# Kernel optimization log

Hardware: AMD Instinct MI355X
Metric: run time of the kernel (lower is better)

Reference implementation:

```python
import jax, jax.numpy as jnp
import numpy as np

WINDOW = (2, 7, 7)
SHIFT = (1, 3, 3)
HEADS = 4


def _rel_pos_index(ws):
    coords = np.stack(np.meshgrid(*[np.arange(w) for w in ws], indexing='ij'))  # (3, wd, wh, ww)
    cf = coords.reshape(3, -1)
    rel = cf[:, :, None] - cf[:, None, :]  # (3, N, N)
    rel = rel.transpose(1, 2, 0).astype(np.int64)
    rel[:, :, 0] += ws[0] - 1
    rel[:, :, 1] += ws[1] - 1
    rel[:, :, 2] += ws[2] - 1
    rel[:, :, 0] *= (2 * ws[1] - 1) * (2 * ws[2] - 1)
    rel[:, :, 1] *= 2 * ws[2] - 1
    return rel.sum(-1)  # (N, N)


def _attn_mask(D, H, W, ws, ss):
    img = np.zeros((1, D, H, W, 1), np.float32)
    cnt = 0
    for d in (slice(None, -ws[0]), slice(-ws[0], -ss[0]), slice(-ss[0], None)):
        for h in (slice(None, -ws[1]), slice(-ws[1], -ss[1]), slice(-ss[1], None)):
            for w in (slice(None, -ws[2]), slice(-ws[2], -ss[2]), slice(-ss[2], None)):
                img[:, d, h, w, :] = cnt
                cnt += 1
    N = ws[0] * ws[1] * ws[2]
    mw = img.reshape(1, D // ws[0], ws[0], H // ws[1], ws[1], W // ws[2], ws[2], 1)
    mw = mw.transpose(0, 1, 3, 5, 2, 4, 6, 7).reshape(-1, N)  # (nW, N)
    diff = mw[:, None, :] - mw[:, :, None]
    return np.where(diff != 0, -100.0, 0.0).astype(np.float32)  # (nW, N, N)


def _win_partition(x, ws):
    B, D, H, W, C = x.shape
    x = x.reshape(B, D // ws[0], ws[0], H // ws[1], ws[1], W // ws[2], ws[2], C)
    return x.transpose(0, 1, 3, 5, 2, 4, 6, 7).reshape(-1, ws[0] * ws[1] * ws[2], C)


def _win_reverse(win, ws, B, D, H, W):
    C = win.shape[-1]
    x = win.reshape(B, D // ws[0], H // ws[1], W // ws[2], ws[0], ws[1], ws[2], C)
    return x.transpose(0, 1, 4, 2, 5, 3, 6, 7).reshape(B, D, H, W, C)


def _ln(x, w, b):
    mu = x.mean(-1, keepdims=True)
    var = x.var(-1, keepdims=True)
    return (x - mu) / jnp.sqrt(var + 1e-5) * w + b


def setup_inputs() -> dict:
    key = jax.random.key(0)
    ks = jax.random.split(key, 8)
    B, D, H, W, C = 4, 8, 56, 56, 128
    hidden = 4 * C
    table = (2 * WINDOW[0] - 1) * (2 * WINDOW[1] - 1) * (2 * WINDOW[2] - 1)
    return {
        'x': jax.random.normal(ks[0], (B, D, H, W, C), jnp.float32),
        'norm1_w': jnp.ones((C,), jnp.float32),
        'norm1_b': jnp.zeros((C,), jnp.float32),
        'qkv_w': 0.02 * jax.random.normal(ks[1], (3 * C, C), jnp.float32),
        'qkv_b': jnp.zeros((3 * C,), jnp.float32),
        'rpb': 0.02 * jax.random.normal(ks[2], (table, HEADS), jnp.float32),
        'proj_w': 0.02 * jax.random.normal(ks[3], (C, C), jnp.float32),
        'proj_b': jnp.zeros((C,), jnp.float32),
        'norm2_w': jnp.ones((C,), jnp.float32),
        'norm2_b': jnp.zeros((C,), jnp.float32),
        'fc1_w': 0.02 * jax.random.normal(ks[4], (hidden, C), jnp.float32),
        'fc1_b': jnp.zeros((hidden,), jnp.float32),
        'fc2_w': 0.02 * jax.random.normal(ks[5], (C, hidden), jnp.float32),
        'fc2_b': jnp.zeros((C,), jnp.float32),
    }


def reference(x, norm1_w, norm1_b, qkv_w, qkv_b, rpb, proj_w, proj_b,
              norm2_w, norm2_b, fc1_w, fc1_b, fc2_w, fc2_b):
    B, D, H, W, C = x.shape
    hd = C // HEADS
    scale = hd ** -0.5
    N = WINDOW[0] * WINDOW[1] * WINDOW[2]

    shortcut = x
    y = _ln(x, norm1_w, norm1_b)
    # cyclic shift (SW-MSA)
    y = jnp.roll(y, (-SHIFT[0], -SHIFT[1], -SHIFT[2]), axis=(1, 2, 3))
    win = _win_partition(y, WINDOW)  # (B_, N, C)
    B_ = win.shape[0]

    qkv = win @ qkv_w.T + qkv_b  # (B_, N, 3C)
    qkv = qkv.reshape(B_, N, 3, HEADS, hd).transpose(2, 0, 3, 1, 4)
    q, k, v = qkv[0] * scale, qkv[1], qkv[2]  # (B_, h, N, hd)

    attn = jnp.einsum('bhnd,bhmd->bhnm', q, k)  # (B_, h, N, N)
    rpi = _rel_pos_index(WINDOW)
    bias = rpb[rpi.reshape(-1)].reshape(N, N, HEADS).transpose(2, 0, 1)  # (h, N, N)
    attn = attn + bias[None]

    mask = jnp.asarray(_attn_mask(D, H, W, WINDOW, SHIFT))  # (nW, N, N)
    nW = mask.shape[0]
    attn = attn.reshape(B_ // nW, nW, HEADS, N, N) + mask[None, :, None]
    attn = jax.nn.softmax(attn.reshape(B_, HEADS, N, N), axis=-1)

    out = jnp.einsum('bhnm,bhmd->bhnd', attn, v)
    out = out.transpose(0, 2, 1, 3).reshape(B_, N, C)
    out = out @ proj_w.T + proj_b

    y = _win_reverse(out, WINDOW, B, D, H, W)
    y = jnp.roll(y, SHIFT, axis=(1, 2, 3))  # reverse cyclic shift
    x = shortcut + y

    h = _ln(x, norm2_w, norm2_b)
    h = jax.nn.gelu(h @ fc1_w.T + fc1_b, approximate=False)
    h = h @ fc2_w.T + fc2_b
    return x + h
```

## Files before the change

kernel.cpp:

```cpp
#include <hip/hip_runtime.h>
#include <math.h>

typedef short bf16x8 __attribute__((ext_vector_type(8)));
typedef float f32x4 __attribute__((ext_vector_type(4)));
typedef unsigned short u16;

#define DEVFN static __device__ __forceinline__

DEVFN u16 f2bf(float f) {
  union { float f; unsigned u; } v; v.f = f;
  return (u16)((v.u + 0x7FFFu + ((v.u >> 16) & 1u)) >> 16);
}

DEVFN void gload16(const void* g, void* l) {
  __builtin_amdgcn_global_load_lds(
      (const __attribute__((address_space(1))) void*)g,
      (__attribute__((address_space(3))) void*)l, 16, 0, 0);
}

DEVFN float gelu_tanh(float x) {
  float x2 = x * x;
  float m = x * fmaf(0.044715f, x2, 1.0f);
  float e = __expf(-1.5957691216057308f * m);
  return x / (1.0f + e);
}

#define TT 100352
#define BWIN 1024

__global__ void convert4_kernel(const float* __restrict__ a, const float* __restrict__ b,
                                const float* __restrict__ c, const float* __restrict__ d,
                                u16* __restrict__ oa, u16* __restrict__ ob,
                                u16* __restrict__ oc, u16* __restrict__ od) {
  int i = blockIdx.x * 256 + threadIdx.x;
  const float* s; u16* o; int off;
  if (i < 49152)       { s = a; o = oa; off = i; }
  else if (i < 65536)  { s = b; o = ob; off = i - 49152; }
  else if (i < 131072) { s = c; o = oc; off = i - 65536; }
  else                 { s = d; o = od; off = i - 131072; }
  o[off] = f2bf(s[off]);
}

__global__ void bias_kernel(const float* __restrict__ rpb, float* __restrict__ bias_full) {
  int idx = blockIdx.x * 256 + threadIdx.x;
  if (idx >= 4 * 9604) return;
  int h = idx / 9604, rem = idx % 9604, i = rem / 98, j = rem % 98;
  int di = i / 49, ri = i % 49, hi = ri / 7, wi = ri % 7;
  int dj = j / 49, rj = j % 49, hj = rj / 7, wj = rj % 7;
  int tidx = (di - dj + 1) * 169 + (hi - hj + 6) * 13 + (wi - wj + 6);
  bias_full[idx] = rpb[tidx * 4 + h];
}

template<int SHIFTED>
__global__ __launch_bounds__(256) void ln_kernel(const float* __restrict__ x,
    const float* __restrict__ w, const float* __restrict__ bterm, u16* __restrict__ out)
{
  int gw = blockIdx.x * 4 + (threadIdx.x >> 6);
  int lane = threadIdx.x & 63;
  size_t src;
  if (SHIFTED) {
    int b_ = gw / 98, n = gw % 98;
    int bb = b_ >> 8, widx = b_ & 255;
    int dw = widx >> 6, hw = (widx >> 3) & 7, ww = widx & 7;
    int dd = n / 49, rr = n % 49, hh = rr / 7, wn = rr % 7;
    int d = (dw * 2 + dd + 1) & 7;
    int h = hw * 7 + hh + 3; if (h >= 56) h -= 56;
    int wq = ww * 7 + wn + 3; if (wq >= 56) wq -= 56;
    src = ((size_t)(((bb * 8 + d) * 56 + h) * 56 + wq)) * 128;
  } else {
    src = (size_t)gw * 128;
  }
  float2 v = *(const float2*)(x + src + lane * 2);
  float s = v.x + v.y, q = v.x * v.x + v.y * v.y;
  #pragma unroll
  for (int m = 1; m < 64; m <<= 1) { s += __shfl_xor(s, m, 64); q += __shfl_xor(q, m, 64); }
  float mu = s * (1.0f / 128.0f);
  float var = q * (1.0f / 128.0f) - mu * mu;
  float rstd = rsqrtf(var + 1e-5f);
  int c = lane * 2;
  float y0 = (v.x - mu) * rstd * w[c] + bterm[c];
  float y1 = (v.y - mu) * rstd * w[c + 1] + bterm[c + 1];
  ushort2 o; o.x = f2bf(y0); o.y = f2bf(y1);
  *(ushort2*)(out + (size_t)gw * 128 + c) = o;
}

template<int EPI>
__global__ __launch_bounds__(256) void gemm_kernel(
    const u16* __restrict__ A, const u16* __restrict__ Bw,
    const float* __restrict__ bias, const float* __restrict__ res,
    void* __restrict__ outp, int M, int N, int K)
{
  __shared__ u16 smem[16384];
  u16* As = smem;
  u16* Bs = smem + 8192;
  const int m0 = blockIdx.x * 128, n0 = blockIdx.y * 128;
  const int t = threadIdx.x;
  const int wid = t >> 6, lane = t & 63;
  const int wr = wid >> 1, wc = wid & 1;
  const int l15 = lane & 15, lhi = lane >> 4;
  const int srow = lane >> 3;
  const int sslot = lane & 7;
  const int gcol = ((sslot ^ srow) << 3);
  f32x4 acc[4][4] = {};
  for (int k0 = 0; k0 < K; k0 += 64) {
    #pragma unroll
    for (int it = 0; it < 4; ++it) {
      const int rbase = it * 32 + wid * 8;
      const int row = rbase + srow;
      gload16(A + (size_t)(m0 + row) * K + k0 + gcol, As + rbase * 64);
      gload16(Bw + (size_t)(n0 + row) * K + k0 + gcol, Bs + rbase * 64);
    }
    __syncthreads();
    #pragma unroll
    for (int kk = 0; kk < 64; kk += 32) {
      bf16x8 af[4], bfr[4];
      const int csw = (kk + lhi * 8) ^ ((l15 & 7) << 3);
      #pragma unroll
      for (int mi = 0; mi < 4; ++mi) af[mi] = *(const bf16x8*)(As + (wr * 64 + mi * 16 + l15) * 64 + csw);
      #pragma unroll
      for (int ni = 0; ni < 4; ++ni) bfr[ni] = *(const bf16x8*)(Bs + (wc * 64 + ni * 16 + l15) * 64 + csw);
      #pragma unroll
      for (int mi = 0; mi < 4; ++mi)
        #pragma unroll
        for (int ni = 0; ni < 4; ++ni)
          acc[mi][ni] = __builtin_amdgcn_mfma_f32_16x16x32_bf16(af[mi], bfr[ni], acc[mi][ni], 0, 0, 0);
    }
    __syncthreads();
  }
  if (EPI == 0) {
    const float smul = (n0 == 0) ? 0.17677669529663689f : 1.0f;
    #pragma unroll
    for (int mi = 0; mi < 4; ++mi)
      #pragma unroll
      for (int ni = 0; ni < 4; ++ni) {
        int col = wc * 64 + ni * 16 + l15;
        float bcol = bias[n0 + col];
        #pragma unroll
        for (int r = 0; r < 4; ++r) {
          int row = wr * 64 + mi * 16 + lhi * 4 + r;
          float v = (acc[mi][ni][r] + bcol) * smul;
          smem[row * 128 + (((col >> 3) ^ (row & 7)) << 3) + (col & 7)] = f2bf(v);
        }
      }
    __syncthreads();
    const int rsub = t >> 4, sl = t & 15;
    #pragma unroll
    for (int j = 0; j < 8; ++j) {
      int row = j * 16 + rsub;
      int4 val = *(const int4*)(smem + row * 128 + ((sl ^ (row & 7)) << 3));
      *(int4*)((u16*)outp + (size_t)(m0 + row) * N + n0 + sl * 8) = val;
    }
  } else {
    #pragma unroll
    for (int mi = 0; mi < 4; ++mi)
      #pragma unroll
      for (int r = 0; r < 4; ++r) {
        int row = m0 + wr * 64 + mi * 16 + lhi * 4 + r;
        int b_ = row / 98, n = row % 98;
        int bb = b_ >> 8, widx = b_ & 255;
        int dw = widx >> 6, hw = (widx >> 3) & 7, ww = widx & 7;
        int dd = n / 49, rr = n % 49, hh = rr / 7, wn = rr % 7;
        int d = (dw * 2 + dd + 1) & 7;
        int h = hw * 7 + hh + 3; if (h >= 56) h -= 56;
        int wq = ww * 7 + wn + 3; if (wq >= 56) wq -= 56;
        size_t dbase = ((size_t)(((bb * 8 + d) * 56 + h) * 56 + wq)) * 128;
        #pragma unroll
        for (int ni = 0; ni < 4; ++ni) {
          int col = n0 + wc * 64 + ni * 16 + l15;
          float v = acc[mi][ni][r] + bias[col];
          ((float*)outp)[dbase + col] = res[dbase + col] + v;
        }
      }
  }
}

__global__ __launch_bounds__(256, 2) void mlp_kernel(
    const u16* __restrict__ A, const u16* __restrict__ W1, const float* __restrict__ b1,
    const u16* __restrict__ W2, const float* __restrict__ b2,
    const float* __restrict__ res, float* __restrict__ outp)
{
  __shared__ u16 smem[38400];
  u16* W1c = smem;
  u16* W2c = smem + 16384;
  u16* HsA = smem + 32768;
  float* b1s = (float*)(smem + 37376);
  float* Pk = (float*)smem;
  const int m0 = blockIdx.x * 64;
  const int t = threadIdx.x, wid = t >> 6, lane = t & 63;
  const int l15 = lane & 15, lhi = lane >> 4;
  const int srow4 = lane >> 4, sslot16 = lane & 15;
  const int srow8 = lane >> 3, sslot8 = lane & 7;
  u16* hs = HsA + wid * 16 * 72;

  #pragma unroll
  for (int it = 0; it < 4; ++it) {
    int rb1 = it * 16 + wid * 4, r1 = rb1 + srow4;
    gload16(W1 + (size_t)r1 * 128 + ((sslot16 ^ (r1 & 7)) << 3), W1c + rb1 * 128);
    int rb2 = it * 32 + wid * 8, r2 = rb2 + srow8;
    gload16(W2 + (size_t)r2 * 512 + ((sslot8 ^ (r2 & 7)) << 3), W2c + rb2 * 64);
  }
  if (t < 128) *(f32x4*)(b1s + t * 4) = *(const f32x4*)(b1 + t * 4);
  bf16x8 areg[4];
  #pragma unroll
  for (int kg = 0; kg < 4; ++kg)
    areg[kg] = *(const bf16x8*)(A + (size_t)(m0 + wid * 16 + l15) * 128 + kg * 32 + lhi * 8);

  f32x4 accO[8] = {};
  __syncthreads();
  for (int hc = 0; hc < 8; ++hc) {
    const int cur = (hc & 1) * 8192;
    if (hc < 7) {
      const int nxt = ((hc + 1) & 1) * 8192;
      #pragma unroll
      for (int it = 0; it < 4; ++it) {
        int rb1 = it * 16 + wid * 4, r1 = rb1 + srow4;
        gload16(W1 + (size_t)((hc + 1) * 64 + r1) * 128 + ((sslot16 ^ (r1 & 7)) << 3),
                W1c + nxt + rb1 * 128);
      }
      #pragma unroll
      for (int it = 0; it < 4; ++it) {
        int rb2 = it * 32 + wid * 8, r2 = rb2 + srow8;
        gload16(W2 + (size_t)r2 * 512 + (hc + 1) * 64 + ((sslot8 ^ (r2 & 7)) << 3),
                W2c + nxt + rb2 * 64);
      }
    }
    f32x4 accH[4] = {};
    #pragma unroll
    for (int kk = 0; kk < 4; ++kk) {
      bf16x8 bfr[4];
      #pragma unroll
      for (int ni = 0; ni < 4; ++ni) {
        int row = ni * 16 + l15;
        bfr[ni] = *(const bf16x8*)(W1c + cur + row * 128 + (((kk * 4 + lhi) ^ (row & 7)) << 3));
      }
      #pragma unroll
      for (int ni = 0; ni < 4; ++ni)
        accH[ni] = __builtin_amdgcn_mfma_f32_16x16x32_bf16(areg[kk], bfr[ni], accH[ni], 0, 0, 0);
    }
    #pragma unroll
    for (int ni = 0; ni < 4; ++ni) {
      float bb = b1s[hc * 64 + ni * 16 + l15];
      #pragma unroll
      for (int r = 0; r < 4; ++r)
        hs[(lhi * 4 + r) * 72 + ni * 16 + l15] = f2bf(gelu_tanh(accH[ni][r] + bb));
    }
    #pragma unroll
    for (int kk = 0; kk < 2; ++kk) {
      bf16x8 ah = *(const bf16x8*)(hs + l15 * 72 + kk * 32 + lhi * 8);
      bf16x8 bfr[8];
      #pragma unroll
      for (int ni = 0; ni < 8; ++ni) {
        int row = ni * 16 + l15;
        bfr[ni] = *(const bf16x8*)(W2c + cur + row * 64 + (((kk * 4 + lhi) ^ (row & 7)) << 3));
      }
      #pragma unroll
      for (int ni = 0; ni < 8; ++ni)
        accO[ni] = __builtin_amdgcn_mfma_f32_16x16x32_bf16(ah, bfr[ni], accO[ni], 0, 0, 0);
    }
    __syncthreads();
  }
  #pragma unroll
  for (int ni = 0; ni < 8; ++ni) {
    int col = ni * 16 + l15;
    float bv = b2[col];
    #pragma unroll
    for (int r = 0; r < 4; ++r)
      Pk[(wid * 16 + lhi * 4 + r) * 132 + col] = accO[ni][r] + bv;
  }
  __syncthreads();
  #pragma unroll
  for (int p = 0; p < 8; ++p) {
    int idx = p * 256 + t;
    int row = idx >> 5, c = (idx & 31) * 4;
    f32x4 v = *(const f32x4*)(Pk + row * 132 + c);
    f32x4 rv = *(const f32x4*)(res + (size_t)(m0 + row) * 128 + c);
    *(f32x4*)(outp + (size_t)(m0 + row) * 128 + c) = v + rv;
  }
}

__global__ __launch_bounds__(64) void attn_kernel(
    const u16* __restrict__ qkv, const float* __restrict__ bias_full,
    u16* __restrict__ out_win)
{
  __shared__ u16 vT[32][136];
  __shared__ u16 P[16][136];
  __shared__ signed char rids[112];
  const int bid = blockIdx.x;
  const int w = bid >> 2, h = bid & 3;
  const int lane = threadIdx.x;
  const int l15 = lane & 15, lhi = lane >> 4;
  const int widx = w & 255;
  const int dw = widx >> 6, hw = (widx >> 3) & 7, ww = widx & 7;

  #pragma unroll
  for (int rep = 0; rep < 2; ++rep) {
    int t2 = lane + rep * 64;
    if (t2 < 112) {
      int rv = 0;
      if (t2 < 98) {
        int dd = t2 / 49, rr = t2 % 49, hh = rr / 7, wn = rr % 7;
        int dp = dw * 2 + dd, hp = hw * 7 + hh, wp = ww * 7 + wn;
        int rd = dp < 6 ? 0 : (dp < 7 ? 1 : 2);
        int rh = hp < 49 ? 0 : (hp < 53 ? 1 : 2);
        int rw2 = wp < 49 ? 0 : (wp < 53 ? 1 : 2);
        rv = rd * 9 + rh * 3 + rw2;
      }
      rids[t2] = (signed char)rv;
    }
  }
  for (int f = lane; f < 160; f += 64) {
    int d = f / 5, c = 96 + (f % 5) * 8;
    *(int4*)&vT[d][c] = (int4){0, 0, 0, 0};
  }
  if (lane < 48) {
    int r = lane / 3, c = 112 + (lane % 3) * 8;
    *(int4*)&P[r][c] = (int4){0, 0, 0, 0};
  }
  const size_t base = (size_t)w * 98 * 384;
  for (int f = lane; f < 392; f += 64) {
    int n = f >> 2, c = (f & 3) * 8;
    int4 v = *(const int4*)(qkv + base + (size_t)n * 384 + 256 + h * 32 + c);
    const u16* pv = (const u16*)&v;
    #pragma unroll
    for (int j = 0; j < 8; ++j) vT[c + j][n] = pv[j];
  }
  __syncthreads();

  const float* bh = bias_full + h * 9604;
  const size_t obase = (size_t)w * 98 * 128;
  for (int mt = 0; mt < 7; ++mt) {
    int qn = mt * 16 + l15; if (qn > 97) qn = 97;
    bf16x8 aq = *(const bf16x8*)(qkv + base + (size_t)qn * 384 + h * 32 + lhi * 8);
    f32x4 sf[7];
    #pragma unroll
    for (int nt = 0; nt < 7; ++nt) {
      int kn = nt * 16 + l15; if (kn > 97) kn = 97;
      bf16x8 bk = *(const bf16x8*)(qkv + base + (size_t)kn * 384 + 128 + h * 32 + lhi * 8);
      f32x4 z = {0.f, 0.f, 0.f, 0.f};
      sf[nt] = __builtin_amdgcn_mfma_f32_16x16x32_bf16(aq, bk, z, 0, 0, 0);
    }
    int irow[4], ridr[4];
    #pragma unroll
    for (int r = 0; r < 4; ++r) {
      irow[r] = mt * 16 + lhi * 4 + r;
      ridr[r] = rids[irow[r] > 111 ? 111 : irow[r]];
    }
    float mx[4] = {-1e30f, -1e30f, -1e30f, -1e30f};
    #pragma unroll
    for (int nt = 0; nt < 7; ++nt) {
      int j = nt * 16 + l15;
      int jc = j > 97 ? 97 : j;
      int rj = rids[j];
      #pragma unroll
      for (int r = 0; r < 4; ++r) {
        float s = sf[nt][r];
        int ic = irow[r] > 97 ? 97 : irow[r];
        s += bh[ic * 98 + jc];
        if (ridr[r] != rj) s -= 100.0f;
        if (j > 97) s = -1e30f;
        sf[nt][r] = s;
        mx[r] = fmaxf(mx[r], s);
      }
    }
    #pragma unroll
    for (int m = 1; m < 16; m <<= 1)
      #pragma unroll
      for (int r = 0; r < 4; ++r) mx[r] = fmaxf(mx[r], __shfl_xor(mx[r], m, 64));
    float sm[4] = {0.f, 0.f, 0.f, 0.f};
    #pragma unroll
    for (int nt = 0; nt < 7; ++nt)
      #pragma unroll
      for (int r = 0; r < 4; ++r) {
        float p = __expf(sf[nt][r] - mx[r]);
        sf[nt][r] = p;
        sm[r] += p;
      }
    #pragma unroll
    for (int m = 1; m < 16; m <<= 1)
      #pragma unroll
      for (int r = 0; r < 4; ++r) sm[r] += __shfl_xor(sm[r], m, 64);
    float inv[4];
    #pragma unroll
    for (int r = 0; r < 4; ++r) inv[r] = 1.0f / sm[r];
    __syncthreads();
    #pragma unroll
    for (int nt = 0; nt < 7; ++nt)
      #pragma unroll
      for (int r = 0; r < 4; ++r)
        P[lhi * 4 + r][nt * 16 + l15] = f2bf(sf[nt][r] * inv[r]);
    __syncthreads();
    f32x4 o0 = {}, o1 = {};
    #pragma unroll
    for (int ks = 0; ks < 4; ++ks) {
      bf16x8 ap  = *(const bf16x8*)(&P[l15][ks * 32 + lhi * 8]);
      bf16x8 bv0 = *(const bf16x8*)(&vT[l15][ks * 32 + lhi * 8]);
      bf16x8 bv1 = *(const bf16x8*)(&vT[16 + l15][ks * 32 + lhi * 8]);
      o0 = __builtin_amdgcn_mfma_f32_16x16x32_bf16(ap, bv0, o0, 0, 0, 0);
      o1 = __builtin_amdgcn_mfma_f32_16x16x32_bf16(ap, bv1, o1, 0, 0, 0);
    }
    #pragma unroll
    for (int r = 0; r < 4; ++r) {
      if (irow[r] < 98) {
        size_t orow = obase + (size_t)irow[r] * 128 + h * 32;
        out_win[orow + l15] = f2bf(o0[r]);
        out_win[orow + 16 + l15] = f2bf(o1[r]);
      }
    }
  }
}

extern "C" void kernel_launch(void* const* d_in, const int* in_sizes, int n_in,
                              void* d_out, int out_size, void* d_ws, size_t ws_size,
                              hipStream_t stream)
{
  const float* x      = (const float*)d_in[0];
  const float* n1w    = (const float*)d_in[1];
  const float* n1b    = (const float*)d_in[2];
  const float* qkv_w  = (const float*)d_in[3];
  const float* qkv_b  = (const float*)d_in[4];
  const float* rpb    = (const float*)d_in[5];
  const float* proj_w = (const float*)d_in[6];
  const float* proj_b = (const float*)d_in[7];
  const float* n2w    = (const float*)d_in[8];
  const float* n2b    = (const float*)d_in[9];
  const float* fc1_w  = (const float*)d_in[10];
  const float* fc1_b  = (const float*)d_in[11];
  const float* fc2_w  = (const float*)d_in[12];
  const float* fc2_b  = (const float*)d_in[13];

  char* p = (char*)d_ws;
  size_t off = 0;
  auto alloc = [&](size_t bytes) { void* r = p + off; off = (off + bytes + 255) & ~(size_t)255; return r; };
  u16*   qkvw_b    = (u16*)alloc(49152 * 2);
  u16*   projw_b   = (u16*)alloc(16384 * 2);
  u16*   fc1w_b    = (u16*)alloc(65536 * 2);
  u16*   fc2w_b    = (u16*)alloc(65536 * 2);
  float* bias_full = (float*)alloc(4 * 9604 * 4);
  u16*   y_win     = (u16*)alloc((size_t)TT * 128 * 2);
  float* x2        = (float*)alloc((size_t)TT * 128 * 4);
  u16*   h1        = (u16*)alloc((size_t)TT * 128 * 2);
  u16*   big       = (u16*)alloc((size_t)TT * 384 * 2);
  if (off > ws_size) return;

  convert4_kernel<<<768, 256, 0, stream>>>(qkv_w, proj_w, fc1_w, fc2_w,
                                           qkvw_b, projw_b, fc1w_b, fc2w_b);
  bias_kernel<<<(4 * 9604 + 255) / 256, 256, 0, stream>>>(rpb, bias_full);
  ln_kernel<1><<<TT / 4, 256, 0, stream>>>(x, n1w, n1b, y_win);
  gemm_kernel<0><<<dim3(TT / 128, 3), 256, 0, stream>>>(y_win, qkvw_b, qkv_b, nullptr, big, TT, 384, 128);
  attn_kernel<<<BWIN * 4, 64, 0, stream>>>(big, bias_full, y_win);
  gemm_kernel<1><<<dim3(TT / 128, 1), 256, 0, stream>>>(y_win, projw_b, proj_b, x, x2, TT, 128, 128);
  ln_kernel<0><<<TT / 4, 256, 0, stream>>>(x2, n2w, n2b, h1);
  mlp_kernel<<<TT / 64, 256, 0, stream>>>(h1, fc1w_b, fc1_b, fc2w_b, fc2_b, x2, (float*)d_out);
}
```

Measured before the change: 234.3 us.

## Double MLP token tile to 128 rows, single-buffer W1, use sigmoid GELU

The fused MLP kernel now handles 128 tokens per block, with each wave owning 32 rows, so every W1/W2 chunk staged in LDS feeds twice as many MFMAs and the grid is halved. To keep LDS small, W1 is single-buffered and its next chunk is prefetched only after a barrier that follows the first GEMM, while W2 stays double-buffered. The epilogue writes the output in two 64-row halves through the same LDS staging area. GELU switches from the tanh form to the cheaper x*sigmoid(1.702x) form using a hardware reciprocal, which is less accurate against the exact erf GELU. The risks are the extra barrier, higher register pressure from doubled accumulators, and less latency hiding on W1.

```diff
diff --git a/kernel.cpp b/kernel.cpp
--- a/kernel.cpp
+++ b/kernel.cpp
@@ -18,11 +18,9 @@
       (__attribute__((address_space(3))) void*)l, 16, 0, 0);
 }
 
-DEVFN float gelu_tanh(float x) {
-  float x2 = x * x;
-  float m = x * fmaf(0.044715f, x2, 1.0f);
-  float e = __expf(-1.5957691216057308f * m);
-  return x / (1.0f + e);
+DEVFN float gelu_fast(float x) {
+  float e = __expf(-1.702f * x);
+  return x * __builtin_amdgcn_rcpf(1.0f + e);
 }
 
 #define TT 100352
@@ -179,18 +177,18 @@
     const u16* __restrict__ W2, const float* __restrict__ b2,
     const float* __restrict__ res, float* __restrict__ outp)
 {
-  __shared__ u16 smem[38400];
+  __shared__ u16 smem[34816];
   u16* W1c = smem;
-  u16* W2c = smem + 16384;
-  u16* HsA = smem + 32768;
-  float* b1s = (float*)(smem + 37376);
+  u16* W2c = smem + 8192;
+  u16* HsA = smem + 24576;
+  float* b1s = (float*)(smem + 33792);
   float* Pk = (float*)smem;
-  const int m0 = blockIdx.x * 64;
+  const int m0 = blockIdx.x * 128;
   const int t = threadIdx.x, wid = t >> 6, lane = t & 63;
   const int l15 = lane & 15, lhi = lane >> 4;
   const int srow4 = lane >> 4, sslot16 = lane & 15;
   const int srow8 = lane >> 3, sslot8 = lane & 7;
-  u16* hs = HsA + wid * 16 * 72;
+  u16* hs = HsA + wid * 2304;
 
   #pragma unroll
   for (int it = 0; it < 4; ++it) {
@@ -200,12 +198,14 @@
     gload16(W2 + (size_t)r2 * 512 + ((sslot8 ^ (r2 & 7)) << 3), W2c + rb2 * 64);
   }
   if (t < 128) *(f32x4*)(b1s + t * 4) = *(const f32x4*)(b1 + t * 4);
-  bf16x8 areg[4];
+  bf16x8 areg[2][4];
   #pragma unroll
-  for (int kg = 0; kg < 4; ++kg)
-    areg[kg] = *(const bf16x8*)(A + (size_t)(m0 + wid * 16 + l15) * 128 + kg * 32 + lhi * 8);
-
-  f32x4 accO[8] = {};
+  for (int mi = 0; mi < 2; ++mi)
+    #pragma unroll
+    for (int kg = 0; kg < 4; ++kg)
+      areg[mi][kg] = *(const bf16x8*)(A + (size_t)(m0 + wid * 32 + mi * 16 + l15) * 128 + kg * 32 + lhi * 8);
+
+  f32x4 accO[2][8] = {};
   __syncthreads();
   for (int hc = 0; hc < 8; ++hc) {
     const int cur = (hc & 1) * 8192;
@@ -213,68 +213,92 @@
       const int nxt = ((hc + 1) & 1) * 8192;
       #pragma unroll
       for (int it = 0; it < 4; ++it) {
-        int rb1 = it * 16 + wid * 4, r1 = rb1 + srow4;
-        gload16(W1 + (size_t)((hc + 1) * 64 + r1) * 128 + ((sslot16 ^ (r1 & 7)) << 3),
-                W1c + nxt + rb1 * 128);
-      }
-      #pragma unroll
-      for (int it = 0; it < 4; ++it) {
         int rb2 = it * 32 + wid * 8, r2 = rb2 + srow8;
         gload16(W2 + (size_t)r2 * 512 + (hc + 1) * 64 + ((sslot8 ^ (r2 & 7)) << 3),
                 W2c + nxt + rb2 * 64);
       }
     }
-    f32x4 accH[4] = {};
+    f32x4 accH[2][4] = {};
     #pragma unroll
     for (int kk = 0; kk < 4; ++kk) {
-      bf16x8 bfr[4];
+      bf16x8 bw[4];
       #pragma unroll
       for (int ni = 0; ni < 4; ++ni) {
         int row = ni * 16 + l15;
-        bfr[ni] = *(const bf16x8*)(W1c + cur + row * 128 + (((kk * 4 + lhi) ^ (row & 7)) << 3));
-      }
-      #pragma unroll
-      for (int ni = 0; ni < 4; ++ni)
-        accH[ni] = __builtin_amdgcn_mfma_f32_16x16x32_bf16(areg[kk], bfr[ni], accH[ni], 0, 0, 0);
-    }
-    #pragma unroll
-    for (int ni = 0; ni < 4; ++ni) {
-      float bb = b1s[hc * 64 + ni * 16 + l15];
-      #pragma unroll
-      for (int r = 0; r < 4; ++r)
-        hs[(lhi * 4 + r) * 72 + ni * 16 + l15] = f2bf(gelu_tanh(accH[ni][r] + bb));
+        bw[ni] = *(const bf16x8*)(W1c + row * 128 + (((kk * 4 + lhi) ^ (row & 7)) << 3));
+      }
+      #pragma unroll
+      for (int mi = 0; mi < 2; ++mi)
+        #pragma unroll
+        for (int ni = 0; ni < 4; ++ni)
+          accH[mi][ni] = __builtin_amdgcn_mfma_f32_16x16x32_bf16(areg[mi][kk], bw[ni], accH[mi][ni], 0, 0, 0);
+    }
+    #pragma unroll
+    for (int mi = 0; mi < 2; ++mi)
+      #pragma unroll
+      for (int ni = 0; ni < 4; ++ni) {
+        float bb = b1s[hc * 64 + ni * 16 + l15];
+        #pragma unroll
+        for (int r = 0; r < 4; ++r) {
+          int tokl = mi * 16 + lhi * 4 + r;
+          hs[tokl * 72 + ni * 16 + l15] = f2bf(gelu_fast(accH[mi][ni][r] + bb));
+        }
+      }
+    __syncthreads();
+    if (hc < 7) {
+      #pragma unroll
+      for (int it = 0; it < 4; ++it) {
+        int rb1 = it * 16 + wid * 4, r1 = rb1 + srow4;
+        gload16(W1 + (size_t)((hc + 1) * 64 + r1) * 128 + ((sslot16 ^ (r1 & 7)) << 3),
+                W1c + rb1 * 128);
+      }
     }
     #pragma unroll
     for (int kk = 0; kk < 2; ++kk) {
-      bf16x8 ah = *(const bf16x8*)(hs + l15 * 72 + kk * 32 + lhi * 8);
-      bf16x8 bfr[8];
+      bf16x8 ah[2], bw2[8];
+      #pragma unroll
+      for (int mi = 0; mi < 2; ++mi)
+        ah[mi] = *(const bf16x8*)(hs + (mi * 16 + l15) * 72 + kk * 32 + lhi * 8);
       #pragma unroll
       for (int ni = 0; ni < 8; ++ni) {
         int row = ni * 16 + l15;
-        bfr[ni] = *(const bf16x8*)(W2c + cur + row * 64 + (((kk * 4 + lhi) ^ (row & 7)) << 3));
-      }
-      #pragma unroll
-      for (int ni = 0; ni < 8; ++ni)
-        accO[ni] = __builtin_amdgcn_mfma_f32_16x16x32_bf16(ah, bfr[ni], accO[ni], 0, 0, 0);
+        bw2[ni] = *(const bf16x8*)(W2c + cur + row * 64 + (((kk * 4 + lhi) ^ (row & 7)) << 3));
+      }
+      #pragma unroll
+      for (int mi = 0; mi < 2; ++mi)
+        #pragma unroll
+        for (int ni = 0; ni < 8; ++ni)
+          accO[mi][ni] = __builtin_amdgcn_mfma_f32_16x16x32_bf16(ah[mi], bw2[ni], accO[mi][ni], 0, 0, 0);
     }
     __syncthreads();
   }
   #pragma unroll
-  for (int ni = 0; ni < 8; ++ni) {
-    int col = ni * 16 + l15;
-    float bv = b2[col];
-    #pragma unroll
-    for (int r = 0; r < 4; ++r)
-      Pk[(wid * 16 + lhi * 4 + r) * 132 + col] = accO[ni][r] + bv;
-  }
-  __syncthreads();
-  #pragma unroll
-  for (int p = 0; p < 8; ++p) {
-    int idx = p * 256 + t;
-    int row = idx >> 5, c = (idx & 31) * 4;
-    f32x4 v = *(const f32x4*)(Pk + row * 132 + c);
-    f32x4 rv = *(const f32x4*)(res + (size_t)(m0 + row) * 128 + c);
-    *(f32x4*)(outp + (size_t)(m0 + row) * 128 + c) = v + rv;
+  for (int half = 0; half < 2; ++half) {
+    if ((wid >> 1) == half) {
+      #pragma unroll
+      for (int ni = 0; ni < 8; ++ni) {
+        int col = ni * 16 + l15;
+        float bv = b2[col];
+        #pragma unroll
+        for (int mi = 0; mi < 2; ++mi)
+          #pragma unroll
+          for (int r = 0; r < 4; ++r) {
+            int tokl = (wid & 1) * 32 + mi * 16 + lhi * 4 + r;
+            Pk[tokl * 132 + col] = accO[mi][ni][r] + bv;
+          }
+      }
+    }
+    __syncthreads();
+    #pragma unroll
+    for (int p = 0; p < 8; ++p) {
+      int idx = p * 256 + t;
+      int row = idx >> 5, c = (idx & 31) * 4;
+      size_t gtok = (size_t)(m0 + half * 64 + row);
+      f32x4 v = *(const f32x4*)(Pk + row * 132 + c);
+      f32x4 rv = *(const f32x4*)(res + gtok * 128 + c);
+      *(f32x4*)(outp + gtok * 128 + c) = v + rv;
+    }
+    __syncthreads();
   }
 }
 
@@ -450,5 +474,5 @@
   attn_kernel<<<BWIN * 4, 64, 0, stream>>>(big, bias_full, y_win);
   gemm_kernel<1><<<dim3(TT / 128, 1), 256, 0, stream>>>(y_win, projw_b, proj_b, x, x2, TT, 128, 128);
   ln_kernel<0><<<TT / 4, 256, 0, stream>>>(x2, n2w, n2b, h1);
-  mlp_kernel<<<TT / 64, 256, 0, stream>>>(h1, fc1w_b, fc1_b, fc2w_b, fc2_b, x2, (float*)d_out);
-}
+  mlp_kernel<<<TT / 128, 256, 0, stream>>>(h1, fc1w_b, fc1_b, fc2w_b, fc2_b, x2, (float*)d_out);
+}
```

After: 220.3 us. -6.0%, faster.
